# Kernel tuning notes

Measured on AMD Instinct MI355X. Metric: run time of the kernel, lower is better.

The kernel has to match this reference:

```python
import jax, jax.numpy as jnp
import numpy as np

N_NODES = 100000
FT_IN = 128
NHID = 64
N_EDGES = 1000000


def setup_inputs() -> dict:
    key = jax.random.key(0)
    ks = jax.random.split(key, 9)
    seq = jax.random.normal(ks[0], (N_NODES, FT_IN), dtype=jnp.float32)
    row = jax.random.randint(ks[1], (N_EDGES,), 0, N_NODES, dtype=jnp.int32)
    col = jax.random.randint(ks[2], (N_EDGES,), 0, N_NODES, dtype=jnp.int32)
    # encoder: LogReg Linear(ft_in, nhid), xavier-uniform weight, zero bias
    lim_enc = float(np.sqrt(6.0 / (FT_IN + NHID)))
    W_enc = jax.random.uniform(ks[3], (NHID, FT_IN), jnp.float32, -lim_enc, lim_enc)
    b_enc = jnp.zeros((NHID,), jnp.float32)
    # decoder lin1: Linear(2*nhid, nhid)
    lim1 = float(1.0 / np.sqrt(2 * NHID))
    W1 = jax.random.uniform(ks[4], (NHID, 2 * NHID), jnp.float32, -lim1, lim1)
    b1 = jax.random.uniform(ks[5], (NHID,), jnp.float32, -lim1, lim1)
    # decoder lin2: Linear(nhid, 1)
    lim2 = float(1.0 / np.sqrt(NHID))
    W2 = jax.random.uniform(ks[6], (1, NHID), jnp.float32, -lim2, lim2)
    b2 = jax.random.uniform(ks[7], (1,), jnp.float32, -lim2, lim2)
    return {"seq": seq, "W_enc": W_enc, "b_enc": b_enc, "W1": W1, "b1": b1,
            "W2": W2, "b2": b2, "row": row, "col": col}


def reference(seq, W_enc, b_enc, W1, b1, W2, b2, row, col):
    # encoder: z_all = seq @ W_enc^T + b_enc   -> [N, nhid]
    z = seq @ W_enc.T + b_enc
    # edge gather + concat -> [E, 2*nhid]
    e = jnp.concatenate([z[row], z[col]], axis=-1)
    h = jax.nn.relu(e @ W1.T + b1)             # [E, nhid]
    out = h @ W2.T + b2                        # [E, 1]
    return out.reshape(-1)
```

## Files before the change

### kernel.cpp

```cpp
#include <hip/hip_runtime.h>
#include <hip/hip_bf16.h>


#define K_IN  128
#define N_OUT 128
#define LDB   136

typedef short bf16x8 __attribute__((ext_vector_type(8)));
typedef float f32x4  __attribute__((ext_vector_type(4)));
typedef _Float16 half8 __attribute__((ext_vector_type(8)));

static __device__ __forceinline__ short f2bf(float x) {
    __hip_bfloat16 h = __float2bfloat16(x);
    return *reinterpret_cast<short*>(&h);
}

__global__ __launch_bounds__(256) void prep_kernel(
        const float* __restrict__ W_enc, const float* __restrict__ b_enc,
        const float* __restrict__ W1,    const float* __restrict__ b1,
        __hip_bfloat16* __restrict__ Wb, float* __restrict__ bcat)
{
    int idx = blockIdx.x * blockDim.x + threadIdx.x;
    if (idx >= N_OUT * K_IN) return;
    int i = idx >> 7;
    int k = idx & 127;
    int irow = i & 63;
    int joff = (i < 64) ? 0 : 64;
    float s = 0.f;
    #pragma unroll 8
    for (int j = 0; j < 64; ++j)
        s = fmaf(W1[irow * 128 + joff + j], W_enc[j * 128 + k], s);
    Wb[i * K_IN + k] = __float2bfloat16(s);
    if (k == 0) {
        float b = 0.f;
        for (int j = 0; j < 64; ++j)
            b = fmaf(W1[irow * 128 + joff + j], b_enc[j], b);
        if (i < 64) b += b1[i];
        bcat[i] = b;
    }
}

__global__ __launch_bounds__(256) void node_proj_kernel(
        const float* __restrict__ seq, const __hip_bfloat16* __restrict__ Wb,
        const float* __restrict__ bcat, _Float16* __restrict__ UVh, int nNodes)
{
    __shared__ short Bs[N_OUT * LDB];

    int tid  = threadIdx.x;
    int base = blockIdx.x * 64;

    #pragma unroll
    for (int it = 0; it < 8; ++it) {
        int c8 = tid + 256 * it;
        int r  = c8 >> 4;
        int cb = (c8 & 15) * 8;
        *(int4*)(Bs + r * LDB + cb) = *(const int4*)(Wb + r * K_IN + cb);
    }
    __syncthreads();

    int lane = tid & 63;
    int w    = tid >> 6;
    int lr   = lane & 15;
    int lg   = lane >> 4;

    int arow = base + 16 * w + lr;
    if (arow >= nNodes) arow = nNodes - 1;
    const float* aptr = seq + (size_t)arow * K_IN + lg * 8;

    f32x4 acc[8];
    #pragma unroll
    for (int nt = 0; nt < 8; ++nt) {
        float b = bcat[nt * 16 + lr];
        acc[nt] = (f32x4){b, b, b, b};
    }

    #pragma unroll
    for (int kk = 0; kk < 4; ++kk) {
        float4 f0 = *(const float4*)(aptr + kk * 32);
        float4 f1 = *(const float4*)(aptr + kk * 32 + 4);
        bf16x8 a;
        a[0] = f2bf(f0.x); a[1] = f2bf(f0.y); a[2] = f2bf(f0.z); a[3] = f2bf(f0.w);
        a[4] = f2bf(f1.x); a[5] = f2bf(f1.y); a[6] = f2bf(f1.z); a[7] = f2bf(f1.w);
        #pragma unroll
        for (int nt = 0; nt < 8; ++nt) {
            bf16x8 b = *(bf16x8*)(Bs + (nt * 16 + lr) * LDB + kk * 32 + lg * 8);
            acc[nt] = __builtin_amdgcn_mfma_f32_16x16x32_bf16(a, b, acc[nt], 0, 0, 0);
        }
    }

    int nodeb = base + 16 * w + lg * 4;
    #pragma unroll
    for (int j = 0; j < 4; ++j) {
        int node = nodeb + j;
        if (node < nNodes) {
            #pragma unroll
            for (int nt = 0; nt < 8; ++nt)
                UVh[(size_t)node * N_OUT + nt * 16 + lr] = (_Float16)acc[nt][j];
        }
    }
}

__global__ __launch_bounds__(256) void edge_kernel(
        const _Float16* __restrict__ UVh, const int* __restrict__ row,
        const int* __restrict__ col, const float* __restrict__ W2,
        const float* __restrict__ b2, float* __restrict__ out, int nEdges)
{
    int l = threadIdx.x & 7;
    float w2v[8];
    #pragma unroll
    for (int j = 0; j < 8; ++j) w2v[j] = W2[l * 8 + j];
    float bb = b2[0];

    int gid = (int)((blockIdx.x * blockDim.x + threadIdx.x) >> 3);
    int ng  = (int)((gridDim.x * blockDim.x) >> 3);

    for (int e0 = gid * 4; e0 < nEdges; e0 += ng * 4) {
        if (e0 + 4 <= nEdges) {
            int4 r4 = *(const int4*)(row + e0);
            int4 c4 = *(const int4*)(col + e0);
            half8 a0 = *(const half8*)(UVh + (size_t)r4.x * N_OUT + l * 8);
            half8 b0 = *(const half8*)(UVh + (size_t)c4.x * N_OUT + 64 + l * 8);
            half8 a1 = *(const half8*)(UVh + (size_t)r4.y * N_OUT + l * 8);
            half8 b1 = *(const half8*)(UVh + (size_t)c4.y * N_OUT + 64 + l * 8);
            half8 a2 = *(const half8*)(UVh + (size_t)r4.z * N_OUT + l * 8);
            half8 b2v = *(const half8*)(UVh + (size_t)c4.z * N_OUT + 64 + l * 8);
            half8 a3 = *(const half8*)(UVh + (size_t)r4.w * N_OUT + l * 8);
            half8 b3 = *(const half8*)(UVh + (size_t)c4.w * N_OUT + 64 + l * 8);

            float p0 = 0.f, p1 = 0.f, p2 = 0.f, p3 = 0.f;
            #pragma unroll
            for (int j = 0; j < 8; ++j) {
                p0 = fmaf(fmaxf((float)a0[j] + (float)b0[j], 0.f), w2v[j], p0);
                p1 = fmaf(fmaxf((float)a1[j] + (float)b1[j], 0.f), w2v[j], p1);
                p2 = fmaf(fmaxf((float)a2[j] + (float)b2v[j], 0.f), w2v[j], p2);
                p3 = fmaf(fmaxf((float)a3[j] + (float)b3[j], 0.f), w2v[j], p3);
            }
            #pragma unroll
            for (int s = 1; s < 8; s <<= 1) {
                p0 += __shfl_xor(p0, s);
                p1 += __shfl_xor(p1, s);
                p2 += __shfl_xor(p2, s);
                p3 += __shfl_xor(p3, s);
            }
            if (l == 0)
                *(float4*)(out + e0) = make_float4(p0 + bb, p1 + bb, p2 + bb, p3 + bb);
        } else {
            for (int e = e0; e < nEdges; ++e) {
                int r = row[e];
                int c = col[e];
                half8 a = *(const half8*)(UVh + (size_t)r * N_OUT + l * 8);
                half8 b = *(const half8*)(UVh + (size_t)c * N_OUT + 64 + l * 8);
                float p = 0.f;
                #pragma unroll
                for (int j = 0; j < 8; ++j)
                    p = fmaf(fmaxf((float)a[j] + (float)b[j], 0.f), w2v[j], p);
                #pragma unroll
                for (int s = 1; s < 8; s <<= 1) p += __shfl_xor(p, s);
                if (l == 0) out[e] = p + bb;
            }
        }
    }
}

extern "C" void kernel_launch(void* const* d_in, const int* in_sizes, int n_in,
                              void* d_out, int out_size, void* d_ws, size_t ws_size,
                              hipStream_t stream) {
    const float* seq   = (const float*)d_in[0];
    const float* W_enc = (const float*)d_in[1];
    const float* b_enc = (const float*)d_in[2];
    const float* W1    = (const float*)d_in[3];
    const float* b1    = (const float*)d_in[4];
    const float* W2    = (const float*)d_in[5];
    const float* b2    = (const float*)d_in[6];
    const int*   row   = (const int*)d_in[7];
    const int*   col   = (const int*)d_in[8];
    float* out = (float*)d_out;

    int nNodes = in_sizes[0] / K_IN;
    int nEdges = in_sizes[7];

    _Float16* UVh = (_Float16*)d_ws;
    __hip_bfloat16* Wb = (__hip_bfloat16*)((char*)d_ws +
                         (size_t)nNodes * N_OUT * sizeof(_Float16));
    float* bcat = (float*)((char*)Wb + N_OUT * K_IN * sizeof(__hip_bfloat16));

    prep_kernel<<<(N_OUT * K_IN + 255) / 256, 256, 0, stream>>>(
        W_enc, b_enc, W1, b1, Wb, bcat);

    int nblocksA = (nNodes + 63) / 64;
    node_proj_kernel<<<nblocksA, 256, 0, stream>>>(seq, Wb, bcat, UVh, nNodes);

    edge_kernel<<<2048, 256, 0, stream>>>(UVh, row, col, W2, b2, out, nEdges);
}
```

Baseline: 59.85 us.

## Drop LDS weight staging, enlarge proj blocks, use nontemporal edge index loads/stores

The node projection kernel no longer copies the bf16 weight matrix into shared memory and instead reads B fragments straight from global memory, relying on cache hits for the small 32KB matrix. It also removes the __syncthreads, and blocks grow to 512 threads covering 128 nodes. The edge kernel loads row/col indices and stores outputs with nontemporal hints so streaming data does not evict the gathered UV table from cache, and it computes gather addresses with 32-bit shifts. Risks include more global/L1 traffic for weights in the projection, and nontemporal hints that may have little effect.

Result: slower. 85.32 us (+42.6%).

```diff
diff --git a/kernel.cpp b/kernel.cpp
--- a/kernel.cpp
+++ b/kernel.cpp
@@ -4,11 +4,12 @@
 
 #define K_IN  128
 #define N_OUT 128
-#define LDB   136
 
 typedef short bf16x8 __attribute__((ext_vector_type(8)));
 typedef float f32x4  __attribute__((ext_vector_type(4)));
 typedef _Float16 half8 __attribute__((ext_vector_type(8)));
+typedef int   i32x4 __attribute__((ext_vector_type(4)));
+typedef float fv4   __attribute__((ext_vector_type(4)));
 
 static __device__ __forceinline__ short f2bf(float x) {
     __hip_bfloat16 h = __float2bfloat16(x);
@@ -40,32 +41,21 @@
     }
 }
 
-__global__ __launch_bounds__(256) void node_proj_kernel(
+__global__ __launch_bounds__(512) void node_proj_kernel(
         const float* __restrict__ seq, const __hip_bfloat16* __restrict__ Wb,
         const float* __restrict__ bcat, _Float16* __restrict__ UVh, int nNodes)
 {
-    __shared__ short Bs[N_OUT * LDB];
-
     int tid  = threadIdx.x;
-    int base = blockIdx.x * 64;
-
-    #pragma unroll
-    for (int it = 0; it < 8; ++it) {
-        int c8 = tid + 256 * it;
-        int r  = c8 >> 4;
-        int cb = (c8 & 15) * 8;
-        *(int4*)(Bs + r * LDB + cb) = *(const int4*)(Wb + r * K_IN + cb);
-    }
-    __syncthreads();
-
     int lane = tid & 63;
     int w    = tid >> 6;
     int lr   = lane & 15;
     int lg   = lane >> 4;
+    int base = blockIdx.x * 128;
 
     int arow = base + 16 * w + lr;
     if (arow >= nNodes) arow = nNodes - 1;
     const float* aptr = seq + (size_t)arow * K_IN + lg * 8;
+    const short* WbS  = (const short*)Wb;
 
     f32x4 acc[8];
     #pragma unroll
@@ -83,7 +73,7 @@
         a[4] = f2bf(f1.x); a[5] = f2bf(f1.y); a[6] = f2bf(f1.z); a[7] = f2bf(f1.w);
         #pragma unroll
         for (int nt = 0; nt < 8; ++nt) {
-            bf16x8 b = *(bf16x8*)(Bs + (nt * 16 + lr) * LDB + kk * 32 + lg * 8);
+            bf16x8 b = *(const bf16x8*)(WbS + (nt * 16 + lr) * K_IN + kk * 32 + lg * 8);
             acc[nt] = __builtin_amdgcn_mfma_f32_16x16x32_bf16(a, b, acc[nt], 0, 0, 0);
         }
     }
@@ -116,16 +106,16 @@
 
     for (int e0 = gid * 4; e0 < nEdges; e0 += ng * 4) {
         if (e0 + 4 <= nEdges) {
-            int4 r4 = *(const int4*)(row + e0);
-            int4 c4 = *(const int4*)(col + e0);
-            half8 a0 = *(const half8*)(UVh + (size_t)r4.x * N_OUT + l * 8);
-            half8 b0 = *(const half8*)(UVh + (size_t)c4.x * N_OUT + 64 + l * 8);
-            half8 a1 = *(const half8*)(UVh + (size_t)r4.y * N_OUT + l * 8);
-            half8 b1 = *(const half8*)(UVh + (size_t)c4.y * N_OUT + 64 + l * 8);
-            half8 a2 = *(const half8*)(UVh + (size_t)r4.z * N_OUT + l * 8);
-            half8 b2v = *(const half8*)(UVh + (size_t)c4.z * N_OUT + 64 + l * 8);
-            half8 a3 = *(const half8*)(UVh + (size_t)r4.w * N_OUT + l * 8);
-            half8 b3 = *(const half8*)(UVh + (size_t)c4.w * N_OUT + 64 + l * 8);
+            i32x4 r4 = __builtin_nontemporal_load((const i32x4*)(row + e0));
+            i32x4 c4 = __builtin_nontemporal_load((const i32x4*)(col + e0));
+            half8 a0 = *(const half8*)(UVh + ((unsigned)r4[0] << 7) + l * 8);
+            half8 b0 = *(const half8*)(UVh + ((unsigned)c4[0] << 7) + 64 + l * 8);
+            half8 a1 = *(const half8*)(UVh + ((unsigned)r4[1] << 7) + l * 8);
+            half8 b1 = *(const half8*)(UVh + ((unsigned)c4[1] << 7) + 64 + l * 8);
+            half8 a2 = *(const half8*)(UVh + ((unsigned)r4[2] << 7) + l * 8);
+            half8 b2v = *(const half8*)(UVh + ((unsigned)c4[2] << 7) + 64 + l * 8);
+            half8 a3 = *(const half8*)(UVh + ((unsigned)r4[3] << 7) + l * 8);
+            half8 b3 = *(const half8*)(UVh + ((unsigned)c4[3] << 7) + 64 + l * 8);
 
             float p0 = 0.f, p1 = 0.f, p2 = 0.f, p3 = 0.f;
             #pragma unroll
@@ -142,14 +132,16 @@
                 p2 += __shfl_xor(p2, s);
                 p3 += __shfl_xor(p3, s);
             }
-            if (l == 0)
-                *(float4*)(out + e0) = make_float4(p0 + bb, p1 + bb, p2 + bb, p3 + bb);
+            if (l == 0) {
+                fv4 o = {p0 + bb, p1 + bb, p2 + bb, p3 + bb};
+                __builtin_nontemporal_store(o, (fv4*)(out + e0));
+            }
         } else {
             for (int e = e0; e < nEdges; ++e) {
                 int r = row[e];
                 int c = col[e];
-                half8 a = *(const half8*)(UVh + (size_t)r * N_OUT + l * 8);
-                half8 b = *(const half8*)(UVh + (size_t)c * N_OUT + 64 + l * 8);
+                half8 a = *(const half8*)(UVh + ((unsigned)r << 7) + l * 8);
+                half8 b = *(const half8*)(UVh + ((unsigned)c << 7) + 64 + l * 8);
                 float p = 0.f;
                 #pragma unroll
                 for (int j = 0; j < 8; ++j)
@@ -187,8 +179,8 @@
     prep_kernel<<<(N_OUT * K_IN + 255) / 256, 256, 0, stream>>>(
         W_enc, b_enc, W1, b1, Wb, bcat);
 
-    int nblocksA = (nNodes + 63) / 64;
-    node_proj_kernel<<<nblocksA, 256, 0, stream>>>(seq, Wb, bcat, UVh, nNodes);
+    int nblocksA = (nNodes + 127) / 128;
+    node_proj_kernel<<<nblocksA, 512, 0, stream>>>(seq, Wb, bcat, UVh, nNodes);
 
     edge_kernel<<<2048, 256, 0, stream>>>(UVh, row, col, W2, b2, out, nEdges);
 }
```
